# Kernel tuning notes

Measured on AMD Instinct MI355X. Metric: run time of the kernel, lower is better.

Reference implementation:

```python
import jax, jax.numpy as jnp
import numpy as np

H = 256          # hidden_dim
NH = 4           # num_heads
HD = H // NH     # head_dim = 64
EPS = 1e-5


def _ln(x, g, b):
    m = jnp.mean(x, axis=-1, keepdims=True)
    v = jnp.mean(jnp.square(x - m), axis=-1, keepdims=True)
    return (x - m) * jax.lax.rsqrt(v + EPS) * g + b


def _mha1(q_in, kv_in, in_proj_w, in_proj_b, out_w, out_b):
    # Single-query / single-key multihead attention (seq_len == 1 on both sides).
    # q_in, kv_in: [B, H]
    Wq, Wk, Wv = jnp.split(in_proj_w, 3, axis=0)   # each [H, H]
    bq, bk, bv = jnp.split(in_proj_b, 3, axis=0)
    B = q_in.shape[0]
    q = (q_in @ Wq.T + bq).reshape(B, NH, HD)
    k = (kv_in @ Wk.T + bk).reshape(B, NH, HD)
    v = (kv_in @ Wv.T + bv).reshape(B, NH, HD)
    scores = jnp.sum(q * k, axis=-1, keepdims=True) / jnp.sqrt(jnp.float32(HD))  # [B,NH,1]
    w = jax.nn.softmax(scores, axis=-1)  # softmax over 1 key -> all ones
    out = (w * v).reshape(B, H)
    return out @ out_w.T + out_b


def setup_inputs() -> dict:
    key = jax.random.key(0)
    ks = jax.random.split(key, 16)
    B, BIO, TXT, NC = 65536, 32, 768, 2
    s = lambda n: 1.0 / np.sqrt(n)
    return {
        "bio": jax.random.normal(ks[0], (B, BIO), jnp.float32),
        "text": jax.random.normal(ks[1], (B, TXT), jnp.float32),
        "bio_w": jax.random.normal(ks[2], (H, BIO), jnp.float32) * s(BIO),
        "bio_b": jnp.zeros((H,), jnp.float32),
        "text_w": jax.random.normal(ks[3], (H, TXT), jnp.float32) * s(TXT),
        "text_b": jnp.zeros((H,), jnp.float32),
        "ln_bio_g": jnp.ones((H,), jnp.float32),
        "ln_bio_b": jnp.zeros((H,), jnp.float32),
        "ln_text_g": jnp.ones((H,), jnp.float32),
        "ln_text_b": jnp.zeros((H,), jnp.float32),
        "in_proj_w": jax.random.normal(ks[4], (3 * H, H), jnp.float32) * s(H),
        "in_proj_b": jnp.zeros((3 * H,), jnp.float32),
        "out_w": jax.random.normal(ks[5], (H, H), jnp.float32) * s(H),
        "out_b": jnp.zeros((H,), jnp.float32),
        "cls1_w": jax.random.normal(ks[6], (H, 2 * H), jnp.float32) * s(2 * H),
        "cls1_b": jnp.zeros((H,), jnp.float32),
        "cls_ln_g": jnp.ones((H,), jnp.float32),
        "cls_ln_b": jnp.zeros((H,), jnp.float32),
        "cls2_w": jax.random.normal(ks[7], (NC, H), jnp.float32) * s(H),
        "cls2_b": jnp.zeros((NC,), jnp.float32),
    }


def reference(bio, text, bio_w, bio_b, text_w, text_b, ln_bio_g, ln_bio_b,
              ln_text_g, ln_text_b, in_proj_w, in_proj_b, out_w, out_b,
              cls1_w, cls1_b, cls_ln_g, cls_ln_b, cls2_w, cls2_b):
    b = _ln(bio @ bio_w.T + bio_b, ln_bio_g, ln_bio_b)      # [B, H]
    t = _ln(text @ text_w.T + text_b, ln_text_g, ln_text_b)  # [B, H]
    attn_bio = _mha1(b, t, in_proj_w, in_proj_b, out_w, out_b)
    attn_text = _mha1(t, b, in_proj_w, in_proj_b, out_w, out_b)
    fused = jnp.concatenate([attn_bio, attn_text], axis=-1)  # [B, 2H]
    h = jax.nn.relu(_ln(fused @ cls1_w.T + cls1_b, cls_ln_g, cls_ln_b))
    return h @ cls2_w.T + cls2_b
```

## Files before the change

### kernel.cpp

```cpp
#include <hip/hip_runtime.h>

typedef __attribute__((ext_vector_type(4))) float f4;
typedef __attribute__((ext_vector_type(8))) short s8;

#define EPS 1e-5f

__device__ __forceinline__ unsigned short f2bf(float f) {
    union { float f; unsigned u; } v; v.f = f;
    unsigned u = v.u;
    return (unsigned short)((u + 0x7fffu + ((u >> 16) & 1u)) >> 16);
}
__device__ __forceinline__ unsigned pack2(float a, float b) {
    return (unsigned)f2bf(a) | ((unsigned)f2bf(b) << 16);
}
__device__ __forceinline__ s8 pack8(f4 a, f4 b) {
    union { s8 v; unsigned u[4]; } r;
    r.u[0] = pack2(a[0], a[1]); r.u[1] = pack2(a[2], a[3]);
    r.u[2] = pack2(b[0], b[1]); r.u[3] = pack2(b[2], b[3]);
    return r.v;
}

__global__ __launch_bounds__(256) void k_prep1(const float* __restrict__ text_w,
                                               const float* __restrict__ bio_w,
                                               const float* __restrict__ out_w,
                                               const float* __restrict__ in_proj_w,
                                               const float* __restrict__ in_proj_b,
                                               const float* __restrict__ out_b,
                                               unsigned short* __restrict__ twFL,
                                               unsigned short* __restrict__ bwFL,
                                               float* __restrict__ A,
                                               float* __restrict__ cvec) {
    int b = blockIdx.x, t = threadIdx.x;
    if (b < 96) {
        int idx = b * 256 + t;
        int ksg = idx >> 10;
        int rem = idx & 1023;
        int ct = rem >> 6, lane = rem & 63;
        int n  = ct * 16 + (lane & 15);
        int k0 = ksg * 32 + ((lane >> 4) << 3);
        const float* src = &text_w[n * 768 + k0];
        f4 a = *(const f4*)src, c = *(const f4*)(src + 4);
        unsigned* dst = (unsigned*)&twFL[idx * 8];
        dst[0] = pack2(a[0], a[1]); dst[1] = pack2(a[2], a[3]);
        dst[2] = pack2(c[0], c[1]); dst[3] = pack2(c[2], c[3]);
    } else if (b < 100) {
        int idx = (b - 96) * 256 + t;
        int ct = idx >> 6, lane = idx & 63;
        int n  = ct * 16 + (lane & 15);
        int k0 = (lane >> 4) << 3;
        const float* src = &bio_w[n * 32 + k0];
        f4 a = *(const f4*)src, c = *(const f4*)(src + 4);
        unsigned* dst = (unsigned*)&bwFL[idx * 8];
        dst[0] = pack2(a[0], a[1]); dst[1] = pack2(a[2], a[3]);
        dst[2] = pack2(c[0], c[1]); dst[3] = pack2(c[2], c[3]);
    } else {
        __shared__ float srow[256];
        __shared__ float red[256];
        int i = b - 100, j = t;
        srow[j] = out_w[i * 256 + j];
        __syncthreads();
        float acc = 0.f;
#pragma unroll 16
        for (int k = 0; k < 256; k++)
            acc = fmaf(srow[k], in_proj_w[(512 + k) * 256 + j], acc);
        A[i * 256 + j] = acc;
        red[j] = srow[j] * in_proj_b[512 + j];
        __syncthreads();
        for (int s = 128; s > 0; s >>= 1) {
            if (j < s) red[j] += red[j + s];
            __syncthreads();
        }
        if (j == 0) cvec[i] = red[0] + out_b[i];
    }
}

__global__ __launch_bounds__(256) void k_prep_PQ(const float* __restrict__ cls1_w,
                                                 const float* __restrict__ cls1_b,
                                                 const float* __restrict__ A,
                                                 const float* __restrict__ cvec,
                                                 const float* __restrict__ ln_text_g,
                                                 const float* __restrict__ ln_text_b,
                                                 const float* __restrict__ ln_bio_g,
                                                 const float* __restrict__ ln_bio_b,
                                                 unsigned short* __restrict__ pqFL,
                                                 float* __restrict__ dvec) {
    __shared__ float w1[256], w2[256], red[256];
    int i = blockIdx.x, j = threadIdx.x;
    w1[j] = cls1_w[i * 512 + j];
    w2[j] = cls1_w[i * 512 + 256 + j];
    __syncthreads();
    float rp = 0.f, rq = 0.f;
#pragma unroll 8
    for (int k = 0; k < 256; k++) {
        float a = A[k * 256 + j];
        rp = fmaf(w1[k], a, rp);
        rq = fmaf(w2[k], a, rq);
    }
    int ct   = i >> 4;
    int lane = (i & 15) | (((j >> 3) & 3) << 4);
    int jj   = j & 7;
    int ks1  = j >> 5;
    pqFL[(((ks1     ) * 16 + ct) * 64 + lane) * 8 + jj] = f2bf(rp * ln_text_g[j]);
    pqFL[(((ks1 + 8 ) * 16 + ct) * 64 + lane) * 8 + jj] = f2bf(rq * ln_bio_g[j]);
    red[j] = rp * ln_text_b[j] + rq * ln_bio_b[j] + (w1[j] + w2[j]) * cvec[j];
    __syncthreads();
    for (int s = 128; s > 0; s >>= 1) {
        if (j < s) red[j] += red[j + s];
        __syncthreads();
    }
    if (j == 0) dvec[i] = red[0] + cls1_b[i];
}

__global__ __launch_bounds__(512, 4) void k_main(
    const float* __restrict__ bio, const float* __restrict__ text,
    const float* __restrict__ bio_b, const float* __restrict__ text_b,
    const float* __restrict__ cls_ln_g, const float* __restrict__ cls_ln_b,
    const float* __restrict__ cls2_w, const float* __restrict__ cls2_b,
    const unsigned short* __restrict__ twFL, const unsigned short* __restrict__ bwFL,
    const unsigned short* __restrict__ pqFL, const float* __restrict__ dvec,
    float* __restrict__ out)
{
    __shared__ __align__(16) unsigned short s_n[64][520];
    __shared__ float s_red[4][64][2];

    const int tid  = threadIdx.x;
    const int wv   = tid >> 6;
    const int cs   = wv & 3;
    const int rh   = wv >> 2;
    const int lane = tid & 63;
    const int q    = lane >> 4;
    const int lr   = lane & 15;
    const int R0   = blockIdx.x * 64;

    f4 acc[2][4];
    float s1[2][4], s2[2][4], m_[2][4], iv_[2][4];

    f4 bioA[2], bioB[2];
#pragma unroll
    for (int rt = 0; rt < 2; rt++) {
        const float* p = &bio[(size_t)(R0 + rh * 32 + rt * 16 + lr) * 32 + q * 8];
        bioA[rt] = *(const f4*)p;
        bioB[rt] = *(const f4*)(p + 4);
    }
    s8 bfrb[4];
#pragma unroll
    for (int c = 0; c < 4; c++)
        bfrb[c] = *(const s8*)&bwFL[((cs * 4 + c) * 64 + lane) * 8];

    int toff[6], soff[6];
    f4 tpre[6];
#pragma unroll
    for (int i = 0; i < 6; i++) {
        int idx = tid + i * 512;
        int row = idx / 48;
        int c4  = idx - row * 48;
        toff[i] = (R0 + row) * 768 + c4 * 4;
        soff[i] = row * 520 + c4 * 4;
        tpre[i] = *(const f4*)&text[(size_t)toff[i]];
    }

#pragma unroll
    for (int rt = 0; rt < 2; rt++)
#pragma unroll
        for (int c = 0; c < 4; c++) acc[rt][c] = (f4){0.f, 0.f, 0.f, 0.f};
#pragma unroll
    for (int rt = 0; rt < 2; rt++) {
        s8 af = pack8(bioA[rt], bioB[rt]);
#pragma unroll
        for (int c = 0; c < 4; c++)
            acc[rt][c] = __builtin_amdgcn_mfma_f32_16x16x32_bf16(af, bfrb[c], acc[rt][c], 0, 0, 0);
    }
#pragma unroll
    for (int rt = 0; rt < 2; rt++)
#pragma unroll
        for (int r = 0; r < 4; r++) { s1[rt][r] = 0.f; s2[rt][r] = 0.f; }
#pragma unroll
    for (int rt = 0; rt < 2; rt++)
#pragma unroll
        for (int c = 0; c < 4; c++) {
            float bb = bio_b[cs * 64 + c * 16 + lr];
#pragma unroll
            for (int r = 0; r < 4; r++) {
                float x = acc[rt][c][r] + bb;
                acc[rt][c][r] = x;
                s1[rt][r] += x; s2[rt][r] += x * x;
            }
        }
#pragma unroll
    for (int off = 1; off < 16; off <<= 1)
#pragma unroll
        for (int rt = 0; rt < 2; rt++)
#pragma unroll
            for (int r = 0; r < 4; r++) {
                s1[rt][r] += __shfl_xor(s1[rt][r], off, 64);
                s2[rt][r] += __shfl_xor(s2[rt][r], off, 64);
            }
    if (lr == 0)
#pragma unroll
        for (int rt = 0; rt < 2; rt++)
#pragma unroll
            for (int r = 0; r < 4; r++) {
                int row = rh * 32 + rt * 16 + q * 4 + r;
                s_red[cs][row][0] = s1[rt][r];
                s_red[cs][row][1] = s2[rt][r];
            }
    __syncthreads();
#pragma unroll
    for (int rt = 0; rt < 2; rt++)
#pragma unroll
        for (int r = 0; r < 4; r++) {
            int row = rh * 32 + rt * 16 + q * 4 + r;
            float t1 = s_red[0][row][0] + s_red[1][row][0] + s_red[2][row][0] + s_red[3][row][0];
            float t2 = s_red[0][row][1] + s_red[1][row][1] + s_red[2][row][1] + s_red[3][row][1];
            float mm = t1 * (1.f / 256.f);
            float vv = t2 * (1.f / 256.f) - mm * mm;
            m_[rt][r]  = mm;
            iv_[rt][r] = rsqrtf(vv + EPS);
        }
#pragma unroll
    for (int rt = 0; rt < 2; rt++)
#pragma unroll
        for (int c = 0; c < 4; c++) {
            int col = cs * 64 + c * 16 + lr;
#pragma unroll
            for (int r = 0; r < 4; r++)
                s_n[rh * 32 + rt * 16 + q * 4 + r][256 + col] =
                    f2bf((acc[rt][c][r] - m_[rt][r]) * iv_[rt][r]);
        }

#pragma unroll
    for (int rt = 0; rt < 2; rt++)
#pragma unroll
        for (int c = 0; c < 4; c++) acc[rt][c] = (f4){0.f, 0.f, 0.f, 0.f};

    for (int ch = 0; ch < 4; ch++) {
        if (ch) __syncthreads();
#pragma unroll
        for (int i = 0; i < 6; i++) {
            uint2 p; p.x = pack2(tpre[i][0], tpre[i][1]); p.y = pack2(tpre[i][2], tpre[i][3]);
            *(uint2*)&((unsigned short*)s_n)[soff[i]] = p;
        }
        if (ch < 3)
#pragma unroll
            for (int i = 0; i < 6; i++)
                tpre[i] = *(const f4*)&text[(size_t)(toff[i] + (ch + 1) * 192)];
        __syncthreads();
        int ksg0 = ch * 6;
#pragma unroll
        for (int ks = 0; ks < 6; ks++) {
            s8 bfr[4];
#pragma unroll
            for (int c = 0; c < 4; c++)
                bfr[c] = *(const s8*)&twFL[(((ksg0 + ks) * 16 + cs * 4 + c) * 64 + lane) * 8];
#pragma unroll
            for (int rt = 0; rt < 2; rt++) {
                s8 af = *(const s8*)&s_n[rh * 32 + rt * 16 + lr][ks * 32 + q * 8];
#pragma unroll
                for (int c = 0; c < 4; c++)
                    acc[rt][c] = __builtin_amdgcn_mfma_f32_16x16x32_bf16(af, bfr[c], acc[rt][c], 0, 0, 0);
            }
        }
    }
#pragma unroll
    for (int rt = 0; rt < 2; rt++)
#pragma unroll
        for (int r = 0; r < 4; r++) { s1[rt][r] = 0.f; s2[rt][r] = 0.f; }
#pragma unroll
    for (int rt = 0; rt < 2; rt++)
#pragma unroll
        for (int c = 0; c < 4; c++) {
            float bb = text_b[cs * 64 + c * 16 + lr];
#pragma unroll
            for (int r = 0; r < 4; r++) {
                float x = acc[rt][c][r] + bb;
                acc[rt][c][r] = x;
                s1[rt][r] += x; s2[rt][r] += x * x;
            }
        }
#pragma unroll
    for (int off = 1; off < 16; off <<= 1)
#pragma unroll
        for (int rt = 0; rt < 2; rt++)
#pragma unroll
            for (int r = 0; r < 4; r++) {
                s1[rt][r] += __shfl_xor(s1[rt][r], off, 64);
                s2[rt][r] += __shfl_xor(s2[rt][r], off, 64);
            }
    __syncthreads();
    if (lr == 0)
#pragma unroll
        for (int rt = 0; rt < 2; rt++)
#pragma unroll
            for (int r = 0; r < 4; r++) {
                int row = rh * 32 + rt * 16 + q * 4 + r;
                s_red[cs][row][0] = s1[rt][r];
                s_red[cs][row][1] = s2[rt][r];
            }
    __syncthreads();
#pragma unroll
    for (int rt = 0; rt < 2; rt++)
#pragma unroll
        for (int r = 0; r < 4; r++) {
            int row = rh * 32 + rt * 16 + q * 4 + r;
            float t1 = s_red[0][row][0] + s_red[1][row][0] + s_red[2][row][0] + s_red[3][row][0];
            float t2 = s_red[0][row][1] + s_red[1][row][1] + s_red[2][row][1] + s_red[3][row][1];
            float mm = t1 * (1.f / 256.f);
            float vv = t2 * (1.f / 256.f) - mm * mm;
            m_[rt][r]  = mm;
            iv_[rt][r] = rsqrtf(vv + EPS);
        }
#pragma unroll
    for (int rt = 0; rt < 2; rt++)
#pragma unroll
        for (int c = 0; c < 4; c++) {
            int col = cs * 64 + c * 16 + lr;
#pragma unroll
            for (int r = 0; r < 4; r++)
                s_n[rh * 32 + rt * 16 + q * 4 + r][col] =
                    f2bf((acc[rt][c][r] - m_[rt][r]) * iv_[rt][r]);
        }
    __syncthreads();

#pragma unroll
    for (int rt = 0; rt < 2; rt++)
#pragma unroll
        for (int c = 0; c < 4; c++) {
            float dv = dvec[cs * 64 + c * 16 + lr];
            acc[rt][c] = (f4){dv, dv, dv, dv};
        }
#pragma unroll 4
    for (int ks = 0; ks < 16; ks++) {
        s8 bfr[4];
#pragma unroll
        for (int c = 0; c < 4; c++)
            bfr[c] = *(const s8*)&pqFL[((ks * 16 + cs * 4 + c) * 64 + lane) * 8];
#pragma unroll
        for (int rt = 0; rt < 2; rt++) {
            s8 af = *(const s8*)&s_n[rh * 32 + rt * 16 + lr][ks * 32 + q * 8];
#pragma unroll
            for (int c = 0; c < 4; c++)
                acc[rt][c] = __builtin_amdgcn_mfma_f32_16x16x32_bf16(af, bfr[c], acc[rt][c], 0, 0, 0);
        }
    }

#pragma unroll
    for (int rt = 0; rt < 2; rt++)
#pragma unroll
        for (int r = 0; r < 4; r++) { s1[rt][r] = 0.f; s2[rt][r] = 0.f; }
#pragma unroll
    for (int rt = 0; rt < 2; rt++)
#pragma unroll
        for (int c = 0; c < 4; c++)
#pragma unroll
            for (int r = 0; r < 4; r++) {
                float x = acc[rt][c][r];
                s1[rt][r] += x; s2[rt][r] += x * x;
            }
#pragma unroll
    for (int off = 1; off < 16; off <<= 1)
#pragma unroll
        for (int rt = 0; rt < 2; rt++)
#pragma unroll
            for (int r = 0; r < 4; r++) {
                s1[rt][r] += __shfl_xor(s1[rt][r], off, 64);
                s2[rt][r] += __shfl_xor(s2[rt][r], off, 64);
            }
    __syncthreads();
    if (lr == 0)
#pragma unroll
        for (int rt = 0; rt < 2; rt++)
#pragma unroll
            for (int r = 0; r < 4; r++) {
                int row = rh * 32 + rt * 16 + q * 4 + r;
                s_red[cs][row][0] = s1[rt][r];
                s_red[cs][row][1] = s2[rt][r];
            }
    __syncthreads();
#pragma unroll
    for (int rt = 0; rt < 2; rt++)
#pragma unroll
        for (int r = 0; r < 4; r++) {
            int row = rh * 32 + rt * 16 + q * 4 + r;
            float t1 = s_red[0][row][0] + s_red[1][row][0] + s_red[2][row][0] + s_red[3][row][0];
            float t2 = s_red[0][row][1] + s_red[1][row][1] + s_red[2][row][1] + s_red[3][row][1];
            float mm = t1 * (1.f / 256.f);
            float vv = t2 * (1.f / 256.f) - mm * mm;
            m_[rt][r]  = mm;
            iv_[rt][r] = rsqrtf(vv + EPS);
        }
    float po0[2][4], po1[2][4];
#pragma unroll
    for (int rt = 0; rt < 2; rt++)
#pragma unroll
        for (int r = 0; r < 4; r++) { po0[rt][r] = 0.f; po1[rt][r] = 0.f; }
#pragma unroll
    for (int rt = 0; rt < 2; rt++)
#pragma unroll
        for (int c = 0; c < 4; c++) {
            int col = cs * 64 + c * 16 + lr;
            float gg = cls_ln_g[col], bb = cls_ln_b[col];
            float c0 = cls2_w[col],   c1 = cls2_w[256 + col];
#pragma unroll
            for (int r = 0; r < 4; r++) {
                float h = fmaxf((acc[rt][c][r] - m_[rt][r]) * iv_[rt][r] * gg + bb, 0.f);
                po0[rt][r] = fmaf(h, c0, po0[rt][r]);
                po1[rt][r] = fmaf(h, c1, po1[rt][r]);
            }
        }
#pragma unroll
    for (int off = 1; off < 16; off <<= 1)
#pragma unroll
        for (int rt = 0; rt < 2; rt++)
#pragma unroll
            for (int r = 0; r < 4; r++) {
                po0[rt][r] += __shfl_xor(po0[rt][r], off, 64);
                po1[rt][r] += __shfl_xor(po1[rt][r], off, 64);
            }
    __syncthreads();
    if (lr == 0)
#pragma unroll
        for (int rt = 0; rt < 2; rt++)
#pragma unroll
            for (int r = 0; r < 4; r++) {
                int row = rh * 32 + rt * 16 + q * 4 + r;
                s_red[cs][row][0] = po0[rt][r];
                s_red[cs][row][1] = po1[rt][r];
            }
    __syncthreads();
    if (tid < 128) {
        int row = tid >> 1, comp = tid & 1;
        float v = s_red[0][row][comp] + s_red[1][row][comp] +
                  s_red[2][row][comp] + s_red[3][row][comp];
        out[(size_t)(R0 + row) * 2 + comp] = v + cls2_b[comp];
    }
}

extern "C" void kernel_launch(void* const* d_in, const int* in_sizes, int n_in,
                              void* d_out, int out_size, void* d_ws, size_t ws_size,
                              hipStream_t stream) {
    const float* bio       = (const float*)d_in[0];
    const float* text      = (const float*)d_in[1];
    const float* bio_w     = (const float*)d_in[2];
    const float* bio_b     = (const float*)d_in[3];
    const float* text_w    = (const float*)d_in[4];
    const float* text_b    = (const float*)d_in[5];
    const float* ln_bio_g  = (const float*)d_in[6];
    const float* ln_bio_b  = (const float*)d_in[7];
    const float* ln_text_g = (const float*)d_in[8];
    const float* ln_text_b = (const float*)d_in[9];
    const float* in_proj_w = (const float*)d_in[10];
    const float* in_proj_b = (const float*)d_in[11];
    const float* out_w     = (const float*)d_in[12];
    const float* out_b     = (const float*)d_in[13];
    const float* cls1_w    = (const float*)d_in[14];
    const float* cls1_b    = (const float*)d_in[15];
    const float* cls_ln_g  = (const float*)d_in[16];
    const float* cls_ln_b  = (const float*)d_in[17];
    const float* cls2_w    = (const float*)d_in[18];
    const float* cls2_b    = (const float*)d_in[19];
    float* out = (float*)d_out;

    float* ws   = (float*)d_ws;
    float* A    = ws;
    float* cvec = ws + 65536;
    float* dvec = ws + 65792;
    unsigned short* us   = (unsigned short*)(ws + 66048);
    unsigned short* twFL = us;
    unsigned short* bwFL = us + 196608;
    unsigned short* pqFL = us + 204800;

    k_prep1  <<<356, 256, 0, stream>>>(text_w, bio_w, out_w, in_proj_w, in_proj_b, out_b,
                                       twFL, bwFL, A, cvec);
    k_prep_PQ<<<256, 256, 0, stream>>>(cls1_w, cls1_b, A, cvec,
                                       ln_text_g, ln_text_b, ln_bio_g, ln_bio_b,
                                       pqFL, dvec);

    int nrows = in_sizes[0] / 32;
    k_main<<<nrows / 64, 512, 0, stream>>>(bio, text, bio_b, text_b,
                                           cls_ln_g, cls_ln_b, cls2_w, cls2_b,
                                           twFL, bwFL, pqFL, dvec, out);
}
```

Measured before the change: 397.3 us.

## Load text activations directly into MFMA fragments, skipping LDS staging

Replaces the cooperative chunked staging of text rows into shared memory (with two barriers per chunk) with each wave loading its own A fragments straight from global memory. A one-step register prefetch overlaps the next loads with the current MFMAs. This removes the LDS writes, reads and syncs, but the text matrix is now read by each of the four column-split waves separately (four times per block instead of once), and per-lane loads are less coalesced (32-byte pieces per row).

```diff
diff --git a/kernel.cpp b/kernel.cpp
--- a/kernel.cpp
+++ b/kernel.cpp
@@ -135,40 +135,29 @@
     f4 acc[2][4];
     float s1[2][4], s2[2][4], m_[2][4], iv_[2][4];
 
-    f4 bioA[2], bioB[2];
-#pragma unroll
-    for (int rt = 0; rt < 2; rt++) {
-        const float* p = &bio[(size_t)(R0 + rh * 32 + rt * 16 + lr) * 32 + q * 8];
-        bioA[rt] = *(const f4*)p;
-        bioB[rt] = *(const f4*)(p + 4);
-    }
-    s8 bfrb[4];
-#pragma unroll
-    for (int c = 0; c < 4; c++)
-        bfrb[c] = *(const s8*)&bwFL[((cs * 4 + c) * 64 + lane) * 8];
-
-    int toff[6], soff[6];
-    f4 tpre[6];
-#pragma unroll
-    for (int i = 0; i < 6; i++) {
-        int idx = tid + i * 512;
-        int row = idx / 48;
-        int c4  = idx - row * 48;
-        toff[i] = (R0 + row) * 768 + c4 * 4;
-        soff[i] = row * 520 + c4 * 4;
-        tpre[i] = *(const f4*)&text[(size_t)toff[i]];
-    }
-
-#pragma unroll
-    for (int rt = 0; rt < 2; rt++)
-#pragma unroll
-        for (int c = 0; c < 4; c++) acc[rt][c] = (f4){0.f, 0.f, 0.f, 0.f};
-#pragma unroll
-    for (int rt = 0; rt < 2; rt++) {
-        s8 af = pack8(bioA[rt], bioB[rt]);
+    {
+        f4 bioA[2], bioB[2];
+#pragma unroll
+        for (int rt = 0; rt < 2; rt++) {
+            const float* p = &bio[(size_t)(R0 + rh * 32 + rt * 16 + lr) * 32 + q * 8];
+            bioA[rt] = *(const f4*)p;
+            bioB[rt] = *(const f4*)(p + 4);
+        }
+        s8 bfrb[4];
 #pragma unroll
         for (int c = 0; c < 4; c++)
-            acc[rt][c] = __builtin_amdgcn_mfma_f32_16x16x32_bf16(af, bfrb[c], acc[rt][c], 0, 0, 0);
+            bfrb[c] = *(const s8*)&bwFL[((cs * 4 + c) * 64 + lane) * 8];
+#pragma unroll
+        for (int rt = 0; rt < 2; rt++)
+#pragma unroll
+            for (int c = 0; c < 4; c++) acc[rt][c] = (f4){0.f, 0.f, 0.f, 0.f};
+#pragma unroll
+        for (int rt = 0; rt < 2; rt++) {
+            s8 af = pack8(bioA[rt], bioB[rt]);
+#pragma unroll
+            for (int c = 0; c < 4; c++)
+                acc[rt][c] = __builtin_amdgcn_mfma_f32_16x16x32_bf16(af, bfrb[c], acc[rt][c], 0, 0, 0);
+        }
     }
 #pragma unroll
     for (int rt = 0; rt < 2; rt++)
@@ -232,33 +221,33 @@
     for (int rt = 0; rt < 2; rt++)
 #pragma unroll
         for (int c = 0; c < 4; c++) acc[rt][c] = (f4){0.f, 0.f, 0.f, 0.f};
-
-    for (int ch = 0; ch < 4; ch++) {
-        if (ch) __syncthreads();
-#pragma unroll
-        for (int i = 0; i < 6; i++) {
-            uint2 p; p.x = pack2(tpre[i][0], tpre[i][1]); p.y = pack2(tpre[i][2], tpre[i][3]);
-            *(uint2*)&((unsigned short*)s_n)[soff[i]] = p;
-        }
-        if (ch < 3)
-#pragma unroll
-            for (int i = 0; i < 6; i++)
-                tpre[i] = *(const f4*)&text[(size_t)(toff[i] + (ch + 1) * 192)];
-        __syncthreads();
-        int ksg0 = ch * 6;
-#pragma unroll
-        for (int ks = 0; ks < 6; ks++) {
+    {
+        const float* tb0 = &text[(size_t)(R0 + rh * 32 + lr) * 768 + q * 8];
+        const float* tb1 = tb0 + 16 * 768;
+        f4 a0lo = *(const f4*)tb0, a0hi = *(const f4*)(tb0 + 4);
+        f4 a1lo = *(const f4*)tb1, a1hi = *(const f4*)(tb1 + 4);
+        for (int ks = 0; ks < 24; ks++) {
+            f4 n0lo, n0hi, n1lo, n1hi;
+            if (ks < 23) {
+                const float* p0 = tb0 + (ks + 1) * 32;
+                const float* p1 = tb1 + (ks + 1) * 32;
+                n0lo = *(const f4*)p0; n0hi = *(const f4*)(p0 + 4);
+                n1lo = *(const f4*)p1; n1hi = *(const f4*)(p1 + 4);
+            }
             s8 bfr[4];
 #pragma unroll
             for (int c = 0; c < 4; c++)
-                bfr[c] = *(const s8*)&twFL[(((ksg0 + ks) * 16 + cs * 4 + c) * 64 + lane) * 8];
-#pragma unroll
-            for (int rt = 0; rt < 2; rt++) {
-                s8 af = *(const s8*)&s_n[rh * 32 + rt * 16 + lr][ks * 32 + q * 8];
-#pragma unroll
-                for (int c = 0; c < 4; c++)
-                    acc[rt][c] = __builtin_amdgcn_mfma_f32_16x16x32_bf16(af, bfr[c], acc[rt][c], 0, 0, 0);
-            }
+                bfr[c] = *(const s8*)&twFL[((ks * 16 + cs * 4 + c) * 64 + lane) * 8];
+            {
+                s8 af0 = pack8(a0lo, a0hi);
+                s8 af1 = pack8(a1lo, a1hi);
+#pragma unroll
+                for (int c = 0; c < 4; c++) {
+                    acc[0][c] = __builtin_amdgcn_mfma_f32_16x16x32_bf16(af0, bfr[c], acc[0][c], 0, 0, 0);
+                    acc[1][c] = __builtin_amdgcn_mfma_f32_16x16x32_bf16(af1, bfr[c], acc[1][c], 0, 0, 0);
+                }
+            }
+            a0lo = n0lo; a0hi = n0hi; a1lo = n1lo; a1hi = n1hi;
         }
     }
 #pragma unroll
```

New measurement: 448.5 us. 12.9% more time.
